# Performance work log

Measured on AMD Instinct MI355X. Metric: run time of the kernel, lower is better.

Reference implementation:

```python
import jax, jax.numpy as jnp
import numpy as np

DIM = 1024
H = 16          # num_heads
D = DIM // H    # head_dim = 64
HID = H * D
N, T = 2, 1024


def setup_inputs() -> dict:
    key = jax.random.key(0)
    ks = jax.random.split(key, 6)
    x = jax.random.normal(ks[0], (N, T, DIM), dtype=jnp.float32)
    # torch nn.Linear stores weight as (out_features, in_features); y = x @ W.T + b
    key_w = jax.random.normal(ks[1], (HID, DIM), dtype=jnp.float32) * DIM ** -0.5
    key_b = jax.random.uniform(ks[2], (HID,), minval=-4.0, maxval=4.0, dtype=jnp.float32)
    vq_w = jax.random.normal(ks[3], (2 * HID, DIM), dtype=jnp.float32) * DIM ** -0.5
    out_w = jax.random.normal(ks[4], (DIM, HID), dtype=jnp.float32) * HID ** -0.5
    out_b = jax.random.normal(ks[5], (DIM,), dtype=jnp.float32) * 0.02
    return {"x": x, "key_w": key_w, "key_b": key_b, "vq_w": vq_w,
            "out_w": out_w, "out_b": out_b}


def reference(x, key_w, key_b, vq_w, out_w, out_b):
    n, t, dim = x.shape
    # projections
    vq = x @ vq_w.T                      # (N,T,2*HID), no bias
    v, q = jnp.split(vq, 2, axis=-1)     # chunk order: v first, q second
    k = jax.nn.sigmoid(x @ key_w.T + key_b)  # (N,T,HID)
    k = k.reshape(n, t, H, D)
    v = v.reshape(n, t, H, D)
    # outer-product update: upd[i,j] = (1-k_i) * v_j  -> (N,T,H,D,D)
    upd = (1.0 - k)[..., :, None] * v[..., None, :]
    # decay per row i is k_i (repeat_interleave over last dim in torch ==
    # broadcasting k over the trailing D axis here)
    decay = k[..., :, None]              # (N,T,H,D,1), broadcasts over j

    # linear recurrence kv_t = decay_t * kv_{t-1} + upd_t via associative scan
    def combine(c1, c2):
        a1, b1 = c1
        a2, b2 = c2
        return (a1 * a2, b1 * a2 + b2)

    _, kv = jax.lax.associative_scan(combine, (decay, upd), axis=1)
    # kv: (N,T,H,D,D)

    qh = q.reshape(n, t, H, D)
    # outer_query_values=False: h = q @ kv, q is (...,1,D) row vector
    h = jnp.einsum('nthd,nthde->nthe', qh, kv).reshape(n, t, HID)
    return h @ out_w.T + out_b
```

## Files before the change

kernel.cpp:

```cpp
#include <hip/hip_runtime.h>
#include <hip/hip_bf16.h>

typedef __attribute__((ext_vector_type(8))) short short8;
typedef __attribute__((ext_vector_type(4))) float f32x4;

constexpr int DIM_ = 1024;
constexpr int H_   = 16;
constexpr int D_   = 64;
constexpr int HID_ = 1024;
constexpr int N_   = 2;
constexpr int T_   = 1024;
constexpr int MTOT = N_ * T_;

constexpr int LC = 32;
constexpr int NC = T_ / LC;
constexpr int NHEAD = N_ * H_;

__device__ __forceinline__ unsigned short f2bf(float f) {
    __hip_bfloat16 h = __float2bfloat16(f);
    unsigned short u; __builtin_memcpy(&u, &h, 2); return u;
}
__device__ __forceinline__ float bf2f(unsigned short u) {
    unsigned int b = ((unsigned int)u) << 16;
    float f; __builtin_memcpy(&f, &b, 4); return f;
}

__device__ __forceinline__ void gload16(const void* g, void* l) {
    __builtin_amdgcn_global_load_lds(
        (const __attribute__((address_space(1))) void*)g,
        (__attribute__((address_space(3))) void*)l, 16, 0, 0);
}

__global__ __launch_bounds__(256) void cvt_all(
    const float* __restrict__ x,  const float* __restrict__ kw,
    const float* __restrict__ vq, const float* __restrict__ ow,
    unsigned short* __restrict__ Xb, unsigned short* __restrict__ Wb,
    unsigned short* __restrict__ OWb)
{
    int b = blockIdx.x;
    const float* src; unsigned short* dst; int off;
    if      (b < 2048) { src = x;  dst = Xb;                 off = b; }
    else if (b < 3072) { src = kw; dst = Wb;                 off = b - 2048; }
    else if (b < 5120) { src = vq; dst = Wb + 1024 * 1024;   off = b - 3072; }
    else               { src = ow; dst = OWb;                off = b - 5120; }
    size_t i = ((size_t)off * 256 + threadIdx.x) * 4;
    float4 v = *(const float4*)&src[i];
    ushort4 o = { f2bf(v.x), f2bf(v.y), f2bf(v.z), f2bf(v.w) };
    *(ushort4*)&dst[i] = o;
}

#define GEMM_BODY(EPILOGUE)                                                          \
    __shared__ unsigned short As[128 * 32];                                          \
    __shared__ unsigned short Bs[128 * 32];                                          \
    const int tid = threadIdx.x, w = tid >> 6, lane = tid & 63;                      \
    const int wm = w >> 1, wn = w & 1;                                               \
    const int M0 = blockIdx.y * 128, N0 = blockIdx.x * 128;                          \
    const int srow = w * 32 + (lane >> 2);                                           \
    const int kA = (((lane & 3) ^ ((srow >> 1) & 3)) * 8);                           \
    const unsigned short* gA = Ab + (size_t)(M0 + srow) * DIM_ + kA;                 \
    const unsigned short* gB = Bb + (size_t)(N0 + srow) * DIM_ + kA;                 \
    char* lA = (char*)As + w * 2048;                                                 \
    char* lB = (char*)Bs + w * 2048;                                                 \
    const int fr = lane & 15, fc = lane >> 4;                                        \
    const int p  = fc ^ ((fr >> 1) & 3);                                             \
    const int aoff = (wm * 64 + fr) * 64 + p * 16;                                   \
    const int boff = (wn * 64 + fr) * 64 + p * 16;                                   \
    f32x4 acc[4][4] = {};                                                            \
    for (int k0 = 0; k0 < DIM_; k0 += 32) {                                          \
        __syncthreads();                                                             \
        gload16(gA + k0,             lA);                                            \
        gload16(gA + k0 + 16 * DIM_, lA + 1024);                                     \
        gload16(gB + k0,             lB);                                            \
        gload16(gB + k0 + 16 * DIM_, lB + 1024);                                     \
        __syncthreads();                                                             \
        short8 a4[4], b4[4];                                                         \
        _Pragma("unroll")                                                            \
        for (int i = 0; i < 4; ++i) {                                                \
            a4[i] = *(const short8*)((const char*)As + aoff + i * 1024);             \
            b4[i] = *(const short8*)((const char*)Bs + boff + i * 1024);             \
        }                                                                            \
        _Pragma("unroll")                                                            \
        for (int mi = 0; mi < 4; ++mi)                                               \
            _Pragma("unroll")                                                        \
            for (int ni = 0; ni < 4; ++ni)                                           \
                acc[mi][ni] = __builtin_amdgcn_mfma_f32_16x16x32_bf16(               \
                    a4[mi], b4[ni], acc[mi][ni], 0, 0, 0);                           \
    }                                                                                \
    const int cm = M0 + wm * 64 + fc * 4;                                            \
    const int cn = N0 + wn * 64 + fr;                                                \
    EPILOGUE

__global__ __launch_bounds__(256) void gemm_qkv_mfma(
    const unsigned short* __restrict__ Ab,
    const unsigned short* __restrict__ Bb,
    const float* __restrict__ key_b,
    float* __restrict__ Kb,
    unsigned short* __restrict__ Vb,
    unsigned short* __restrict__ Qb)
{
    GEMM_BODY(
        if (N0 < HID_) {
            _Pragma("unroll")
            for (int ni = 0; ni < 4; ++ni) {
                float bias = key_b[cn + ni * 16];
                _Pragma("unroll")
                for (int mi = 0; mi < 4; ++mi)
                    _Pragma("unroll")
                    for (int r = 0; r < 4; ++r) {
                        float vv = acc[mi][ni][r] + bias;
                        Kb[(size_t)(cm + mi * 16 + r) * HID_ + cn + ni * 16] =
                            1.f / (1.f + __expf(-vv));
                    }
            }
        } else if (N0 < 2 * HID_) {
            _Pragma("unroll")
            for (int ni = 0; ni < 4; ++ni)
                _Pragma("unroll")
                for (int mi = 0; mi < 4; ++mi)
                    _Pragma("unroll")
                    for (int r = 0; r < 4; ++r)
                        Vb[(size_t)(cm + mi * 16 + r) * HID_ + cn + ni * 16 - HID_] =
                            f2bf(acc[mi][ni][r]);
        } else {
            _Pragma("unroll")
            for (int ni = 0; ni < 4; ++ni)
                _Pragma("unroll")
                for (int mi = 0; mi < 4; ++mi)
                    _Pragma("unroll")
                    for (int r = 0; r < 4; ++r)
                        Qb[(size_t)(cm + mi * 16 + r) * HID_ + cn + ni * 16 - 2 * HID_] =
                            f2bf(acc[mi][ni][r]);
        }
    )
}

__global__ __launch_bounds__(256) void gemm_out_mfma(
    const unsigned short* __restrict__ Ab,
    const unsigned short* __restrict__ Bb,
    const float* __restrict__ out_b,
    float* __restrict__ Out)
{
    GEMM_BODY(
        _Pragma("unroll")
        for (int ni = 0; ni < 4; ++ni) {
            float bias = out_b[cn + ni * 16];
            _Pragma("unroll")
            for (int mi = 0; mi < 4; ++mi)
                _Pragma("unroll")
                for (int r = 0; r < 4; ++r)
                    Out[(size_t)(cm + mi * 16 + r) * DIM_ + cn + ni * 16] =
                        acc[mi][ni][r] + bias;
        }
    )
}

__global__ __launch_bounds__(256) void scan_phase1(
    const float* __restrict__ Kb,
    const unsigned short* __restrict__ Vb,
    const unsigned short* __restrict__ Qb,
    unsigned short* __restrict__ SbufB,
    float* __restrict__ Pbuf,
    unsigned short* __restrict__ QAb,
    unsigned short* __restrict__ Hb)
{
    __shared__ float sk[LC][64];
    __shared__ float sv[LC][64];
    __shared__ float sq[LC][64];
    __shared__ unsigned short hp[4][16][64];
    __shared__ unsigned short qs[LC][64];

    const int tid  = threadIdx.x;
    const int w    = tid >> 6;
    const int lane = tid & 63;
    const int c    = blockIdx.x & (NC - 1);
    const int head = blockIdx.x >> 5;
    const int n = head >> 4, h = head & 15;
    const size_t base = ((size_t)n * T_) * HID_ + (size_t)h * 64;

    #pragma unroll
    for (int i = 0; i < 2; ++i) {
        int f = tid * 4 + i * 1024;
        int tl = f >> 6, d = f & 63;
        float4 k4 = *(const float4*)&Kb[base + (size_t)(c * LC + tl) * HID_ + d];
        *(float4*)&sk[tl][d] = k4;
    }
    {
        int f = tid * 8;
        int tl = f >> 6, d = f & 63;
        size_t g = base + (size_t)(c * LC + tl) * HID_ + d;
        short8 v8 = *(const short8*)&Vb[g];
        short8 q8 = *(const short8*)&Qb[g];
        #pragma unroll
        for (int j = 0; j < 8; ++j) {
            sv[tl][d + j] = bf2f((unsigned short)v8[j]);
            sq[tl][d + j] = bf2f((unsigned short)q8[j]);
        }
    }
    __syncthreads();

    const int dq = w * 16 + (lane & 15);
    float kv[16];
    #pragma unroll
    for (int i = 0; i < 16; ++i) kv[i] = 0.f;
    float pq = 1.f;

    #pragma unroll
    for (int half = 0; half < 2; ++half) {
        for (int tl2 = 0; tl2 < 16; ++tl2) {
            const int tl = half * 16 + tl2;
            float part = 0.f;
            float v = sv[tl][lane];
            #pragma unroll
            for (int i4 = 0; i4 < 4; ++i4) {
                float4 k4 = *(const float4*)&sk[tl][w * 16 + i4 * 4];
                float4 q4 = *(const float4*)&sq[tl][w * 16 + i4 * 4];
                float ks[4] = {k4.x, k4.y, k4.z, k4.w};
                float qs_[4] = {q4.x, q4.y, q4.z, q4.w};
                #pragma unroll
                for (int j = 0; j < 4; ++j) {
                    int i = i4 * 4 + j;
                    kv[i] = ks[j] * kv[i] + (1.f - ks[j]) * v;
                    part += qs_[j] * kv[i];
                }
            }
            hp[w][tl2][lane] = f2bf(part);
            pq *= sk[tl][dq];
            if (lane < 16) qs[tl][dq] = f2bf(sq[tl][dq] * pq);
        }
        __syncthreads();
        #pragma unroll
        for (int i = 0; i < 16 * 64 / 256; ++i) {
            int idx = tid + i * 256;
            int tl2 = idx >> 6, e = idx & 63;
            float s = bf2f(hp[0][tl2][e]) + bf2f(hp[1][tl2][e]) +
                      bf2f(hp[2][tl2][e]) + bf2f(hp[3][tl2][e]);
            Hb[base + (size_t)(c * LC + half * 16 + tl2) * HID_ + e] = f2bf(s);
        }
        __syncthreads();
    }

    const size_t sbase = (size_t)(head * NC + c) * (D_ * D_);
    #pragma unroll
    for (int i = 0; i < 4; ++i) {
        ushort4 o = { f2bf(kv[i * 4 + 0]), f2bf(kv[i * 4 + 1]),
                      f2bf(kv[i * 4 + 2]), f2bf(kv[i * 4 + 3]) };
        *(ushort4*)&SbufB[sbase + (size_t)lane * D_ + w * 16 + i * 4] = o;
    }
    if (lane < 16) Pbuf[(size_t)(head * NC + c) * D_ + dq] = pq;
    const unsigned short* qsl = &qs[0][0];
    *(short8*)&QAb[(size_t)(head * NC + c) * (LC * 64) + tid * 8] =
        *(const short8*)&qsl[tid * 8];
}

__global__ __launch_bounds__(256) void scan_combine(
    const unsigned short* __restrict__ SbufB,
    const float* __restrict__ Pbuf,
    unsigned short* __restrict__ SInitB)
{
    const int tid  = threadIdx.x;
    const int head = blockIdx.x >> 4;
    const int e    = (blockIdx.x & 15) * 4 + (tid >> 6);
    const int d    = tid & 63;

    float S = 0.f;
    for (int ci = 0; ci < NC; ++ci) {
        const size_t sidx = (size_t)(head * NC + ci) * (D_ * D_) + (size_t)e * D_ + d;
        float B  = bf2f(SbufB[sidx]);
        float pp = Pbuf[(size_t)(head * NC + ci) * D_ + d];
        SInitB[sidx] = f2bf(S);
        S = pp * S + B;
    }
}

__global__ __launch_bounds__(256) void scan_inter_mfma(
    const unsigned short* __restrict__ QAb,
    const unsigned short* __restrict__ SInitB,
    unsigned short* __restrict__ Hb)
{
    const int tid = threadIdx.x, w = tid >> 6, lane = tid & 63;
    const int wid  = blockIdx.x * 4 + w;
    const int head = wid >> 5, c = wid & 31;
    if (c == 0) return;
    const int n = head >> 4, h = head & 15;
    const int fr = lane & 15, fc = lane >> 4;

    const unsigned short* qa = QAb + (size_t)(head * NC + c) * (LC * 64);
    const unsigned short* sb = SInitB + (size_t)(head * NC + c) * (D_ * D_);

    short8 a[2][2], b[4][2];
    #pragma unroll
    for (int mi = 0; mi < 2; ++mi)
        #pragma unroll
        for (int ks = 0; ks < 2; ++ks)
            a[mi][ks] = *(const short8*)&qa[(mi * 16 + fr) * 64 + fc * 8 + ks * 32];
    #pragma unroll
    for (int ni = 0; ni < 4; ++ni)
        #pragma unroll
        for (int ks = 0; ks < 2; ++ks)
            b[ni][ks] = *(const short8*)&sb[(ni * 16 + fr) * 64 + fc * 8 + ks * 32];

    f32x4 acc[2][4] = {};
    #pragma unroll
    for (int mi = 0; mi < 2; ++mi)
        #pragma unroll
        for (int ni = 0; ni < 4; ++ni)
            #pragma unroll
            for (int ks = 0; ks < 2; ++ks)
                acc[mi][ni] = __builtin_amdgcn_mfma_f32_16x16x32_bf16(
                    a[mi][ks], b[ni][ks], acc[mi][ni], 0, 0, 0);

    #pragma unroll
    for (int mi = 0; mi < 2; ++mi)
        #pragma unroll
        for (int ni = 0; ni < 4; ++ni)
            #pragma unroll
            for (int r = 0; r < 4; ++r) {
                int t = c * LC + mi * 16 + fc * 4 + r;
                size_t g = ((size_t)n * T_ + t) * HID_ + h * 64 + ni * 16 + fr;
                Hb[g] = f2bf(bf2f(Hb[g]) + acc[mi][ni][r]);
            }
}

extern "C" void kernel_launch(void* const* d_in, const int* in_sizes, int n_in,
                              void* d_out, int out_size, void* d_ws, size_t ws_size,
                              hipStream_t stream)
{
    const float* x     = (const float*)d_in[0];
    const float* key_w = (const float*)d_in[1];
    const float* key_b = (const float*)d_in[2];
    const float* vq_w  = (const float*)d_in[3];
    const float* out_w = (const float*)d_in[4];
    const float* out_b = (const float*)d_in[5];
    float* out = (float*)d_out;

    const size_t MH = (size_t)MTOT * HID_;
    float* Kb   = (float*)d_ws;
    unsigned short* Vb16  = (unsigned short*)(Kb + MH);
    unsigned short* Qb16  = Vb16 + MH;
    unsigned short* SbufB = Qb16 + MH;
    unsigned short* SInitB = SbufB + (size_t)NHEAD * NC * D_ * D_;
    float* Pbuf = (float*)(SInitB + (size_t)NHEAD * NC * D_ * D_);
    unsigned short* QAb = (unsigned short*)(Pbuf + (size_t)NHEAD * NC * D_);
    unsigned short* Xb  = QAb + (size_t)NHEAD * NC * LC * D_;
    unsigned short* Wb  = Xb + MH;
    unsigned short* OWb = Wb + 3 * 1024 * 1024;
    unsigned short* Hb  = OWb + 1024 * 1024;

    cvt_all<<<6144, 256, 0, stream>>>(x, key_w, vq_w, out_w, Xb, Wb, OWb);
    gemm_qkv_mfma<<<dim3(24, 16), 256, 0, stream>>>(Xb, Wb, key_b, Kb, Vb16, Qb16);
    scan_phase1<<<NHEAD * NC, 256, 0, stream>>>(Kb, Vb16, Qb16, SbufB, Pbuf, QAb, Hb);
    scan_combine<<<NHEAD * 16, 256, 0, stream>>>(SbufB, Pbuf, SInitB);
    scan_inter_mfma<<<NHEAD * NC / 4, 256, 0, stream>>>(QAb, SInitB, Hb);
    gemm_out_mfma<<<dim3(8, 16), 256, 0, stream>>>(Hb, OWb, out_b, out);
}
```

Before: 94.05 us.

## Double-buffer GEMM LDS tiles, swizzle block order, prefetch scan-combine loads

The GEMM main loop now double-buffers its A/B LDS tiles, so the next k-slice load is issued before the MFMAs on the current one and each iteration needs one barrier instead of two. Blocks are remapped through an XCD-aware swizzle of a 1D grid to improve L2 locality. The scan_combine kernel loads all chunk values into registers before the serial recurrence, and the phase1 recurrence is rewritten as FMAs. LDS use per block doubles, which may reduce occupancy.

Result: slower. 96.81 us (+2.9%).

```diff
diff --git a/kernel.cpp b/kernel.cpp
--- a/kernel.cpp
+++ b/kernel.cpp
@@ -49,35 +49,45 @@
     *(ushort4*)&dst[i] = o;
 }
 
-#define GEMM_BODY(EPILOGUE)                                                          \
-    __shared__ unsigned short As[128 * 32];                                          \
-    __shared__ unsigned short Bs[128 * 32];                                          \
+#define GEMM_BODY(NXT, EPILOGUE)                                                     \
+    __shared__ unsigned short As[2][128 * 32];                                       \
+    __shared__ unsigned short Bs[2][128 * 32];                                       \
     const int tid = threadIdx.x, w = tid >> 6, lane = tid & 63;                      \
     const int wm = w >> 1, wn = w & 1;                                               \
-    const int M0 = blockIdx.y * 128, N0 = blockIdx.x * 128;                          \
+    const int nwg = gridDim.x;                                                       \
+    const int cpx = nwg >> 3;                                                        \
+    const int swz = (blockIdx.x & 7) * cpx + (blockIdx.x >> 3);                      \
+    const int M0 = (swz / (NXT)) * 128, N0 = (swz % (NXT)) * 128;                    \
     const int srow = w * 32 + (lane >> 2);                                           \
     const int kA = (((lane & 3) ^ ((srow >> 1) & 3)) * 8);                           \
     const unsigned short* gA = Ab + (size_t)(M0 + srow) * DIM_ + kA;                 \
     const unsigned short* gB = Bb + (size_t)(N0 + srow) * DIM_ + kA;                 \
-    char* lA = (char*)As + w * 2048;                                                 \
-    char* lB = (char*)Bs + w * 2048;                                                 \
+    const int lofs = w * 2048;                                                       \
     const int fr = lane & 15, fc = lane >> 4;                                        \
     const int p  = fc ^ ((fr >> 1) & 3);                                             \
     const int aoff = (wm * 64 + fr) * 64 + p * 16;                                   \
     const int boff = (wn * 64 + fr) * 64 + p * 16;                                   \
     f32x4 acc[4][4] = {};                                                            \
-    for (int k0 = 0; k0 < DIM_; k0 += 32) {                                          \
-        __syncthreads();                                                             \
-        gload16(gA + k0,             lA);                                            \
-        gload16(gA + k0 + 16 * DIM_, lA + 1024);                                     \
-        gload16(gB + k0,             lB);                                            \
-        gload16(gB + k0 + 16 * DIM_, lB + 1024);                                     \
-        __syncthreads();                                                             \
+                                              \
+    gload16(gA,             (char*)As[0] + lofs);                                    \
+    gload16(gA + 16 * DIM_, (char*)As[0] + lofs + 1024);                             \
+    gload16(gB,             (char*)Bs[0] + lofs);                                    \
+    gload16(gB + 16 * DIM_, (char*)Bs[0] + lofs + 1024);                             \
+    __syncthreads();                                                                 \
+    int cur = 0;                                                                     \
+    for (int t = 0; t < DIM_ / 32; ++t) {                                            \
+        if (t < DIM_ / 32 - 1) {                                                     \
+            const int k1 = (t + 1) * 32;                                             \
+            gload16(gA + k1,             (char*)As[cur ^ 1] + lofs);                 \
+            gload16(gA + k1 + 16 * DIM_, (char*)As[cur ^ 1] + lofs + 1024);          \
+            gload16(gB + k1,             (char*)Bs[cur ^ 1] + lofs);                 \
+            gload16(gB + k1 + 16 * DIM_, (char*)Bs[cur ^ 1] + lofs + 1024);          \
+        }                                                                            \
         short8 a4[4], b4[4];                                                         \
         _Pragma("unroll")                                                            \
         for (int i = 0; i < 4; ++i) {                                                \
-            a4[i] = *(const short8*)((const char*)As + aoff + i * 1024);             \
-            b4[i] = *(const short8*)((const char*)Bs + boff + i * 1024);             \
+            a4[i] = *(const short8*)((const char*)As[cur] + aoff + i * 1024);        \
+            b4[i] = *(const short8*)((const char*)Bs[cur] + boff + i * 1024);        \
         }                                                                            \
         _Pragma("unroll")                                                            \
         for (int mi = 0; mi < 4; ++mi)                                               \
@@ -85,6 +95,10 @@
             for (int ni = 0; ni < 4; ++ni)                                           \
                 acc[mi][ni] = __builtin_amdgcn_mfma_f32_16x16x32_bf16(               \
                     a4[mi], b4[ni], acc[mi][ni], 0, 0, 0);                           \
+        if (t < DIM_ / 32 - 1) {                                                     \
+            __syncthreads();                                                         \
+            cur ^= 1;                                                                \
+        }                                                                            \
     }                                                                                \
     const int cm = M0 + wm * 64 + fc * 4;                                            \
     const int cn = N0 + wn * 64 + fr;                                                \
@@ -98,7 +112,7 @@
     unsigned short* __restrict__ Vb,
     unsigned short* __restrict__ Qb)
 {
-    GEMM_BODY(
+    GEMM_BODY(24,
         if (N0 < HID_) {
             _Pragma("unroll")
             for (int ni = 0; ni < 4; ++ni) {
@@ -140,7 +154,7 @@
     const float* __restrict__ out_b,
     float* __restrict__ Out)
 {
-    GEMM_BODY(
+    GEMM_BODY(8,
         _Pragma("unroll")
         for (int ni = 0; ni < 4; ++ni) {
             float bias = out_b[cn + ni * 16];
@@ -219,8 +233,8 @@
                 #pragma unroll
                 for (int j = 0; j < 4; ++j) {
                     int i = i4 * 4 + j;
-                    kv[i] = ks[j] * kv[i] + (1.f - ks[j]) * v;
-                    part += qs_[j] * kv[i];
+                    kv[i] = __builtin_fmaf(ks[j], kv[i] - v, v);
+                    part  = __builtin_fmaf(qs_[j], kv[i], part);
                 }
             }
             hp[w][tl2][lane] = f2bf(part);
@@ -262,13 +276,21 @@
     const int e    = (blockIdx.x & 15) * 4 + (tid >> 6);
     const int d    = tid & 63;
 
-    float S = 0.f;
+    unsigned short Bv[NC];
+    float Pv[NC];
+    #pragma unroll
     for (int ci = 0; ci < NC; ++ci) {
         const size_t sidx = (size_t)(head * NC + ci) * (D_ * D_) + (size_t)e * D_ + d;
-        float B  = bf2f(SbufB[sidx]);
-        float pp = Pbuf[(size_t)(head * NC + ci) * D_ + d];
+        Bv[ci] = SbufB[sidx];
+        Pv[ci] = Pbuf[(size_t)(head * NC + ci) * D_ + d];
+    }
+
+    float S = 0.f;
+    #pragma unroll
+    for (int ci = 0; ci < NC; ++ci) {
+        const size_t sidx = (size_t)(head * NC + ci) * (D_ * D_) + (size_t)e * D_ + d;
         SInitB[sidx] = f2bf(S);
-        S = pp * S + B;
+        S = Pv[ci] * S + bf2f(Bv[ci]);
     }
 }
 
@@ -347,9 +369,9 @@
     unsigned short* Hb  = OWb + 1024 * 1024;
 
     cvt_all<<<6144, 256, 0, stream>>>(x, key_w, vq_w, out_w, Xb, Wb, OWb);
-    gemm_qkv_mfma<<<dim3(24, 16), 256, 0, stream>>>(Xb, Wb, key_b, Kb, Vb16, Qb16);
+    gemm_qkv_mfma<<<384, 256, 0, stream>>>(Xb, Wb, key_b, Kb, Vb16, Qb16);
     scan_phase1<<<NHEAD * NC, 256, 0, stream>>>(Kb, Vb16, Qb16, SbufB, Pbuf, QAb, Hb);
     scan_combine<<<NHEAD * 16, 256, 0, stream>>>(SbufB, Pbuf, SInitB);
     scan_inter_mfma<<<NHEAD * NC / 4, 256, 0, stream>>>(QAb, SInitB, Hb);
-    gemm_out_mfma<<<dim3(8, 16), 256, 0, stream>>>(Hb, OWb, out_b, out);
-}
+    gemm_out_mfma<<<128, 256, 0, stream>>>(Hb, OWb, out_b, out);
+}
```
